# Kernel optimization log

Hardware: AMD Instinct MI355X
Metric: run time of the kernel (lower is better)

Reference implementation:

```python
import jax, jax.numpy as jnp
import numpy as np

NX, NC, E = 100000, 50000, 1000000
DIN, DCTX, DH, DOUT = 64, 64, 64, 64


def _linear_params(k, din, dout):
    kw, _ = jax.random.split(k)
    s = 1.0 / np.sqrt(din).astype(np.float32)
    return jax.random.uniform(kw, (dout, din), jnp.float32, -s, s), jnp.zeros((dout,), jnp.float32)


def setup_inputs() -> dict:
    key = jax.random.key(0)
    ks = jax.random.split(key, 16)
    x = jax.random.normal(ks[0], (NX, DIN), jnp.float32)
    c = jax.random.normal(ks[1], (NC, DCTX), jnp.float32)
    e_fwd_src = jax.random.randint(ks[2], (E,), 0, NX, jnp.int32)
    e_fwd_dst = jax.random.randint(ks[3], (E,), 0, NX, jnp.int32)
    e_bwd_src = jax.random.randint(ks[4], (E,), 0, NX, jnp.int32)
    e_bwd_dst = jax.random.randint(ks[5], (E,), 0, NX, jnp.int32)
    e_cx_src = jax.random.randint(ks[6], (E,), 0, NC, jnp.int32)
    e_cx_dst = jax.random.randint(ks[7], (E,), 0, NX, jnp.int32)
    Wx, bx = _linear_params(ks[8], DIN, DH)      # layers['x']
    Wc, bc = _linear_params(ks[9], DCTX, DH)     # layers['c']
    Wff, bff = _linear_params(ks[10], DIN, DH)   # layers['x->x']
    Wbb, bbb = _linear_params(ks[11], DIN, DH)   # layers['x<-x']
    Wcx, bcx = _linear_params(ks[12], DCTX, DH)  # layers['c->x']
    Wp, bp = _linear_params(ks[13], DH, DOUT)    # pool
    return dict(x=x, c=c,
                e_fwd_src=e_fwd_src, e_fwd_dst=e_fwd_dst,
                e_bwd_src=e_bwd_src, e_bwd_dst=e_bwd_dst,
                e_cx_src=e_cx_src, e_cx_dst=e_cx_dst,
                Wx=Wx, bx=bx, Wc=Wc, bc=bc, Wff=Wff, bff=bff,
                Wbb=Wbb, bbb=bbb, Wcx=Wcx, bcx=bcx, Wp=Wp, bp=bp)


def reference(x, c, e_fwd_src, e_fwd_dst, e_bwd_src, e_bwd_dst, e_cx_src, e_cx_dst,
              Wx, bx, Wc, bc, Wff, bff, Wbb, bbb, Wcx, bcx, Wp, bp):
    relu = jax.nn.relu
    seg = lambda v, i: jax.ops.segment_sum(v, i, num_segments=NX)
    # self-loop features
    self_x = relu(x @ Wx.T + bx)                                   # [NX, DH]
    # edge type ('x','->','x'): gather src, transform, scatter-add to dst
    m1 = seg(relu(x[e_fwd_src] @ Wff.T + bff), e_fwd_dst)
    # edge type ('x','<-','x'): direction swap -> true src is stored dst
    m2 = seg(relu(x[e_bwd_dst] @ Wbb.T + bbb), e_bwd_src)
    # edge type ('c','->','x'): gather context nodes
    m3 = seg(relu(c[e_cx_src] @ Wcx.T + bcx), e_cx_dst)
    # coalesce with op='add' over all messages + self loops
    agg = self_x + m1 + m2 + m3                                    # [NX, DH]
    out_x = agg @ Wp.T + bp                                        # [NX, DOUT]
    out_c = relu(c @ Wc.T + bc)                                    # [NC, DH]
    return out_x, out_c
```

## Files before the change

### kernel.cpp

```cpp
#include <hip/hip_runtime.h>
#include <cstddef>

typedef unsigned short ushort_t;
using f32x4  = __attribute__((ext_vector_type(4))) float;
using bf16x8 = __attribute__((ext_vector_type(8))) short;

static constexpr int NX = 100000;
static constexpr int NC = 50000;
static constexpr int E  = 1000000;
static constexpr int E3 = 3 * E;

static constexpr int SHIFT = 6;
static constexpr int BN = 1 << SHIFT;
static constexpr int NB = (NX + BN - 1) / BN;
static constexpr int CAP = 2304;
static constexpr int PF_CHUNK = 4096;
static constexpr int NXT = (NX + 63) / 64;
static constexpr int NCT = (NC + 63) / 64;

__device__ inline ushort_t f2bf(float f) {
    unsigned u = __float_as_uint(f);
    return (ushort_t)((u + 0x7fffu + ((u >> 16) & 1u)) >> 16);
}

__device__ inline bf16x8 cvt8(float4 lo, float4 hi) {
    bf16x8 v;
    v[0] = (short)f2bf(lo.x); v[1] = (short)f2bf(lo.y);
    v[2] = (short)f2bf(lo.z); v[3] = (short)f2bf(lo.w);
    v[4] = (short)f2bf(hi.x); v[5] = (short)f2bf(hi.y);
    v[6] = (short)f2bf(hi.z); v[7] = (short)f2bf(hi.w);
    return v;
}

__device__ inline float bfl(unsigned u) { return __uint_as_float(u << 16); }
__device__ inline float bfh(unsigned u) { return __uint_as_float(u & 0xffff0000u); }

__device__ __forceinline__ void gemm_tile(
    const float* __restrict__ in, int nrows, int tile_row0,
    const float* __restrict__ W0, const float* __restrict__ b0, void* __restrict__ o0,
    const float* __restrict__ W1, const float* __restrict__ b1, void* __restrict__ o1,
    const float* __restrict__ W2, const float* __restrict__ b2, void* __restrict__ o2,
    int nlayers, int relu_mask, int bf16_mask)
{
    const int t   = threadIdx.x;
    const int w   = t >> 6;
    const int l   = t & 63;
    const int lr  = l & 15;
    const int lk  = (l >> 4) * 8;
    const int row0 = tile_row0 + (w >> 1) * 32;
    const int col0 = (w & 1) * 32;

    bf16x8 a[2][2];
    #pragma unroll
    for (int m = 0; m < 2; ++m) {
        #pragma unroll
        for (int ks = 0; ks < 2; ++ks) {
            const int row = row0 + 16 * m + lr;
            float4 lo = make_float4(0.f, 0.f, 0.f, 0.f), hi = lo;
            if (row < nrows) {
                const float* p = in + (size_t)row * 64 + ks * 32 + lk;
                lo = *reinterpret_cast<const float4*>(p);
                hi = *reinterpret_cast<const float4*>(p + 4);
            }
            a[m][ks] = cvt8(lo, hi);
        }
    }

    for (int ly = 0; ly < nlayers; ++ly) {
        const float* W = (ly == 0) ? W0 : (ly == 1) ? W1 : W2;
        const float* b = (ly == 0) ? b0 : (ly == 1) ? b1 : b2;
        void*        o = (ly == 0) ? o0 : (ly == 1) ? o1 : o2;

        bf16x8 bf[2][2];
        float  bias[2];
        #pragma unroll
        for (int n = 0; n < 2; ++n) {
            const int col = col0 + 16 * n + lr;
            bias[n] = b[col];
            #pragma unroll
            for (int ks = 0; ks < 2; ++ks) {
                const float* p = W + (size_t)col * 64 + ks * 32 + lk;
                const float4 lo = *reinterpret_cast<const float4*>(p);
                const float4 hi = *reinterpret_cast<const float4*>(p + 4);
                bf[n][ks] = cvt8(lo, hi);
            }
        }

        f32x4 acc[2][2];
        #pragma unroll
        for (int m = 0; m < 2; ++m)
            #pragma unroll
            for (int n = 0; n < 2; ++n)
                acc[m][n] = (f32x4){0.f, 0.f, 0.f, 0.f};

        #pragma unroll
        for (int m = 0; m < 2; ++m) {
            #pragma unroll
            for (int n = 0; n < 2; ++n) {
                acc[m][n] = __builtin_amdgcn_mfma_f32_16x16x32_bf16(a[m][0], bf[n][0], acc[m][n], 0, 0, 0);
                acc[m][n] = __builtin_amdgcn_mfma_f32_16x16x32_bf16(a[m][1], bf[n][1], acc[m][n], 0, 0, 0);
            }
        }

        const bool relu = (relu_mask >> ly) & 1;
        const bool b16  = (bf16_mask >> ly) & 1;
        #pragma unroll
        for (int m = 0; m < 2; ++m) {
            #pragma unroll
            for (int r = 0; r < 4; ++r) {
                const int row = row0 + 16 * m + (l >> 4) * 4 + r;
                if (row < nrows) {
                    #pragma unroll
                    for (int n = 0; n < 2; ++n) {
                        const int col = col0 + 16 * n + lr;
                        float v = acc[m][n][r] + bias[n];
                        if (relu) v = fmaxf(v, 0.f);
                        if (b16) ((ushort_t*)o)[(size_t)row * 64 + col] = f2bf(v);
                        else     ((float*)o)[(size_t)row * 64 + col] = v;
                    }
                }
            }
        }
    }
}

__global__ __launch_bounds__(256) void gemm_all(
    const float* __restrict__ x, const float* __restrict__ c,
    const float* __restrict__ Wx, const float* __restrict__ bx, ushort_t* __restrict__ h_self,
    const float* __restrict__ Wff, const float* __restrict__ bff, ushort_t* __restrict__ hff,
    const float* __restrict__ Wbb, const float* __restrict__ bbb, ushort_t* __restrict__ hbb,
    const float* __restrict__ Wc, const float* __restrict__ bc, float* __restrict__ out_c,
    const float* __restrict__ Wcx, const float* __restrict__ bcx, ushort_t* __restrict__ hcx,
    int* __restrict__ bcursor)
{
    const int b = blockIdx.x;
    if (b < NXT) {
        gemm_tile(x, NX, b * 64, Wx, bx, h_self, Wff, bff, hff, Wbb, bbb, hbb, 3, 7, 7);
    } else if (b < NXT + NCT) {
        gemm_tile(c, NC, (b - NXT) * 64, Wc, bc, out_c, Wcx, bcx, hcx,
                  nullptr, nullptr, nullptr, 2, 3, 2);
    } else {
        for (int i = threadIdx.x; i < NB; i += 256) bcursor[i] = i * CAP;
    }
}

__global__ __launch_bounds__(256) void fused_linear_mfma(
    const float* __restrict__ in, int nrows,
    const float* __restrict__ W0, const float* __restrict__ b0, void* __restrict__ o0,
    const float* __restrict__ W1, const float* __restrict__ b1, void* __restrict__ o1,
    const float* __restrict__ W2, const float* __restrict__ b2, void* __restrict__ o2,
    int nlayers, int relu_mask, int bf16_mask)
{
    gemm_tile(in, nrows, blockIdx.x * 64, W0, b0, o0, W1, b1, o1, W2, b2, o2,
              nlayers, relu_mask, bf16_mask);
}

__global__ __launch_bounds__(256) void partition_fill(
    const int* __restrict__ efs, const int* __restrict__ efd,
    const int* __restrict__ ebs, const int* __restrict__ ebd,
    const int* __restrict__ ecs, const int* __restrict__ ecd,
    int* __restrict__ bcursor, unsigned* __restrict__ pk)
{
    __shared__ int h[NB];
    __shared__ int base[NB];
    for (int i = threadIdx.x; i < NB; i += 256) h[i] = 0;
    __syncthreads();
    const int e0 = blockIdx.x * PF_CHUNK;
    unsigned pack[16];
    int buck[16], rank[16];
    #pragma unroll
    for (int i = 0; i < 16; ++i) {
        const int e = e0 + i * 256 + threadIdx.x;
        buck[i] = -1;
        if (e < E3) {
            int d, sg;
            if (e < E)          { d = efd[e];         sg = efs[e]; }
            else if (e < 2 * E) { d = ebs[e - E];     sg = NX + ebd[e - E]; }
            else                { d = ecd[e - 2 * E]; sg = 2 * NX + ecs[e - 2 * E]; }
            buck[i] = d >> SHIFT;
            pack[i] = ((unsigned)sg << SHIFT) | (unsigned)(d & (BN - 1));
            rank[i] = atomicAdd(&h[buck[i]], 1);
        }
    }
    __syncthreads();
    for (int b = threadIdx.x; b < NB; b += 256)
        base[b] = h[b] ? atomicAdd(&bcursor[b], h[b]) : 0;
    __syncthreads();
    #pragma unroll
    for (int i = 0; i < 16; ++i)
        if (buck[i] >= 0) pk[base[buck[i]] + rank[i]] = pack[i];
}

__global__ __launch_bounds__(256) void sort_gather_pool(
    const int* __restrict__ bcursor, const unsigned* __restrict__ pk,
    const ushort_t* __restrict__ h_all, const ushort_t* __restrict__ h_self,
    const float* __restrict__ Wp, const float* __restrict__ bp,
    float* __restrict__ out_x)
{
    __shared__ unsigned srt[CAP];
    __shared__ int cnt[BN], nstart[BN], cur[BN];
    __shared__ ushort_t agg_lds[BN * 72];

    const int b = blockIdx.x;
    const int t = threadIdx.x;
    const int s = b * CAP;
    int tend = bcursor[b];
    if (tend > s + CAP) tend = s + CAP;

    if (t < BN) cnt[t] = 0;
    __syncthreads();
    for (int e = s + t; e < tend; e += 256)
        atomicAdd(&cnt[pk[e] & (BN - 1)], 1);
    __syncthreads();
    if (t < BN) {
        const int v = cnt[t];
        int xs = v;
        #pragma unroll
        for (int d = 1; d < BN; d <<= 1) {
            const int y = __shfl_up(xs, d, 64);
            if (t >= d) xs += y;
        }
        nstart[t] = xs - v;
        cur[t]    = xs - v;
    }
    __syncthreads();
    for (int e = s + t; e < tend; e += 256) {
        const unsigned p = pk[e];
        const int pos = atomicAdd(&cur[p & (BN - 1)], 1);
        srt[pos] = (p & ~(unsigned)(BN - 1)) << 1;
    }
    __syncthreads();

    const int w    = t >> 6;
    const int lane = t & 63;
    const int q    = lane >> 4;
    const int fl   = lane & 15;
    const unsigned foff = fl * 8;
    const int node0 = b * BN;
    const char* hb = reinterpret_cast<const char*>(h_all);
    const char* hs = reinterpret_cast<const char*>(h_self);

    for (int i = 0; i < 16; ++i) {
        const int nl   = w * 16 + i;
        const int node = node0 + nl;
        const int start = nstart[nl];
        const int count = cnt[nl];
        float a0 = 0.f, a1 = 0.f, a2 = 0.f, a3 = 0.f;
        if (q == 0 && node < NX) {
            const uint2 u = *reinterpret_cast<const uint2*>(hs + (size_t)node * 128 + foff);
            a0 = bfl(u.x); a1 = bfh(u.x); a2 = bfl(u.y); a3 = bfh(u.y);
        }
        int e = q;
        for (; e + 12 < count; e += 16) {
            const unsigned o0 = srt[start + e]      + foff;
            const unsigned o1 = srt[start + e + 4]  + foff;
            const unsigned o2 = srt[start + e + 8]  + foff;
            const unsigned o3 = srt[start + e + 12] + foff;
            const uint2 u0 = *reinterpret_cast<const uint2*>(hb + o0);
            const uint2 u1 = *reinterpret_cast<const uint2*>(hb + o1);
            const uint2 u2 = *reinterpret_cast<const uint2*>(hb + o2);
            const uint2 u3 = *reinterpret_cast<const uint2*>(hb + o3);
            a0 += bfl(u0.x) + bfl(u1.x) + bfl(u2.x) + bfl(u3.x);
            a1 += bfh(u0.x) + bfh(u1.x) + bfh(u2.x) + bfh(u3.x);
            a2 += bfl(u0.y) + bfl(u1.y) + bfl(u2.y) + bfl(u3.y);
            a3 += bfh(u0.y) + bfh(u1.y) + bfh(u2.y) + bfh(u3.y);
        }
        for (; e < count; e += 4) {
            const uint2 u = *reinterpret_cast<const uint2*>(hb + (srt[start + e] + foff));
            a0 += bfl(u.x); a1 += bfh(u.x); a2 += bfl(u.y); a3 += bfh(u.y);
        }
        a0 += __shfl_xor(a0, 16); a0 += __shfl_xor(a0, 32);
        a1 += __shfl_xor(a1, 16); a1 += __shfl_xor(a1, 32);
        a2 += __shfl_xor(a2, 16); a2 += __shfl_xor(a2, 32);
        a3 += __shfl_xor(a3, 16); a3 += __shfl_xor(a3, 32);
        if (q == 0) {
            uint2 pck;
            pck.x = ((unsigned)f2bf(a1) << 16) | (unsigned)f2bf(a0);
            pck.y = ((unsigned)f2bf(a3) << 16) | (unsigned)f2bf(a2);
            *reinterpret_cast<uint2*>(&agg_lds[nl * 72 + fl * 4]) = pck;
        }
    }
    __syncthreads();

    const int lr = lane & 15, q4 = lane >> 4;
    const float* wrow = Wp + (size_t)(w * 16 + lr) * 64;
    const bf16x8 bf0 = cvt8(*reinterpret_cast<const float4*>(wrow + q4 * 8),
                            *reinterpret_cast<const float4*>(wrow + q4 * 8 + 4));
    const bf16x8 bf1 = cvt8(*reinterpret_cast<const float4*>(wrow + 32 + q4 * 8),
                            *reinterpret_cast<const float4*>(wrow + 32 + q4 * 8 + 4));
    const float bias = bp[w * 16 + lr];
    #pragma unroll
    for (int rb = 0; rb < 4; ++rb) {
        const bf16x8 af0 = *reinterpret_cast<const bf16x8*>(&agg_lds[(rb * 16 + lr) * 72 + q4 * 8]);
        const bf16x8 af1 = *reinterpret_cast<const bf16x8*>(&agg_lds[(rb * 16 + lr) * 72 + 32 + q4 * 8]);
        f32x4 acc = (f32x4){0.f, 0.f, 0.f, 0.f};
        acc = __builtin_amdgcn_mfma_f32_16x16x32_bf16(af0, bf0, acc, 0, 0, 0);
        acc = __builtin_amdgcn_mfma_f32_16x16x32_bf16(af1, bf1, acc, 0, 0, 0);
        #pragma unroll
        for (int r = 0; r < 4; ++r) {
            const int row = node0 + rb * 16 + q4 * 4 + r;
            if (row < NX)
                out_x[(size_t)row * 64 + w * 16 + lr] = acc[r] + bias;
        }
    }
}

__global__ __launch_bounds__(256) void scatter_edges(
    const int* __restrict__ efs, const int* __restrict__ efd,
    const int* __restrict__ ebs, const int* __restrict__ ebd,
    const int* __restrict__ ecs, const int* __restrict__ ecd,
    const ushort_t* __restrict__ h_all, float* __restrict__ agg)
{
    const int idx  = blockIdx.x * 256 + threadIdx.x;
    const int lane = idx & 63;
    const int e    = idx >> 6;
    if (e >= E3) return;
    int src, dst;
    if (e < E)          { src = efs[e];           dst = efd[e]; }
    else if (e < 2 * E) { src = NX + ebd[e - E];  dst = ebs[e - E]; }
    else                { src = 2 * NX + ecs[e - 2 * E]; dst = ecd[e - 2 * E]; }
    const unsigned u = (unsigned)h_all[(size_t)src * 64 + lane] << 16;
    atomicAdd(&agg[(size_t)dst * 64 + lane], __uint_as_float(u));
}

extern "C" void kernel_launch(void* const* d_in, const int* in_sizes, int n_in,
                              void* d_out, int out_size, void* d_ws, size_t ws_size,
                              hipStream_t stream)
{
    const float* x   = (const float*)d_in[0];
    const float* c   = (const float*)d_in[1];
    const int*   efs = (const int*)d_in[2];
    const int*   efd = (const int*)d_in[3];
    const int*   ebs = (const int*)d_in[4];
    const int*   ebd = (const int*)d_in[5];
    const int*   ecs = (const int*)d_in[6];
    const int*   ecd = (const int*)d_in[7];
    const float* Wx  = (const float*)d_in[8];
    const float* bx  = (const float*)d_in[9];
    const float* Wc  = (const float*)d_in[10];
    const float* bc  = (const float*)d_in[11];
    const float* Wff = (const float*)d_in[12];
    const float* bff = (const float*)d_in[13];
    const float* Wbb = (const float*)d_in[14];
    const float* bbb = (const float*)d_in[15];
    const float* Wcx = (const float*)d_in[16];
    const float* bcx = (const float*)d_in[17];
    const float* Wp  = (const float*)d_in[18];
    const float* bp  = (const float*)d_in[19];

    float* out_x = (float*)d_out;
    float* out_c = (float*)d_out + (size_t)NX * 64;

    ushort_t* h_all  = (ushort_t*)d_ws;
    ushort_t* hff    = h_all;
    ushort_t* hbb    = h_all + (size_t)NX * 64;
    ushort_t* hcx    = h_all + (size_t)2 * NX * 64;
    ushort_t* h_self = h_all + (size_t)(2 * NX + NC) * 64;
    const size_t h_elems = (size_t)(3 * NX + NC) * 64;

    int* bcursor = (int*)(h_all + h_elems);
    unsigned* pk = (unsigned*)(bcursor + NB);
    const size_t need_bytes = h_elems * 2 + (size_t)NB * 4 + (size_t)NB * CAP * 4;

    if (ws_size >= need_bytes) {
        gemm_all<<<NXT + NCT + 1, 256, 0, stream>>>(
            x, c, Wx, bx, h_self, Wff, bff, hff, Wbb, bbb, hbb,
            Wc, bc, out_c, Wcx, bcx, hcx, bcursor);
        partition_fill<<<(E3 + PF_CHUNK - 1) / PF_CHUNK, 256, 0, stream>>>(
            efs, efd, ebs, ebd, ecs, ecd, bcursor, pk);
        sort_gather_pool<<<NB, 256, 0, stream>>>(
            bcursor, pk, h_all, h_self, Wp, bp, out_x);
    } else {
        fused_linear_mfma<<<NXT, 256, 0, stream>>>(
            x, NX, Wx, bx, out_x, Wff, bff, hff, Wbb, bbb, hbb, 3, 7, 6);
        fused_linear_mfma<<<NCT, 256, 0, stream>>>(
            c, NC, Wc, bc, out_c, Wcx, bcx, hcx, nullptr, nullptr, nullptr, 2, 3, 2);
        scatter_edges<<<((size_t)E3 * 64 + 255) / 256, 256, 0, stream>>>(
            efs, efd, ebs, ebd, ecs, ecd, h_all, out_x);
        fused_linear_mfma<<<NXT, 256, 0, stream>>>(
            out_x, NX, Wp, bp, out_x, nullptr, nullptr, nullptr, nullptr, nullptr, nullptr, 1, 0, 0);
    }
}
```

Measured before the change: 151.3 us.

## Use coarser partition buckets with two-pass fill and split gather into quarter-bucket blocks

Partitioning now uses 128-node buckets. The fill kernel makes two passes: it counts first, reserves global cursor ranges, then re-reads the edge indices to scatter packed entries, instead of keeping per-thread ranks in registers. The gather/pool kernel launches four 32-node blocks per parent bucket, interleaved so neighbouring blocks share parent buckets for cache locality. Each block filters the parent's packed list for its quarter. This raises parallelism and lowers per-block shared memory and register pressure. The cost is re-reading edge indices in the fill kernel and each packed bucket being scanned four times.

Result: slower. 179.1 us (+18.3%).

```diff
diff --git a/kernel.cpp b/kernel.cpp
--- a/kernel.cpp
+++ b/kernel.cpp
@@ -10,11 +10,16 @@
 static constexpr int E  = 1000000;
 static constexpr int E3 = 3 * E;
 
-static constexpr int SHIFT = 6;
-static constexpr int BN = 1 << SHIFT;
-static constexpr int NB = (NX + BN - 1) / BN;
-static constexpr int CAP = 2304;
-static constexpr int PF_CHUNK = 4096;
+static constexpr int SHIFT_P = 7;
+static constexpr int BNP = 1 << SHIFT_P;
+static constexpr int NBP = (NX + BNP - 1) / BNP;
+static constexpr int CAP_P = 4416;
+static constexpr int PF_CHUNK = 8192;
+
+static constexpr int BNG = 32;
+static constexpr int CAP_G = 1280;
+static constexpr int GRID_G = 8 * 4 * ((NBP + 7) / 8);
+
 static constexpr int NXT = (NX + 63) / 64;
 static constexpr int NCT = (NC + 63) / 64;
 
@@ -140,7 +145,7 @@
         gemm_tile(c, NC, (b - NXT) * 64, Wc, bc, out_c, Wcx, bcx, hcx,
                   nullptr, nullptr, nullptr, 2, 3, 2);
     } else {
-        for (int i = threadIdx.x; i < NB; i += 256) bcursor[i] = i * CAP;
+        for (int i = threadIdx.x; i < NBP; i += 256) bcursor[i] = i * CAP_P;
     }
 }
 
@@ -161,34 +166,42 @@
     const int* __restrict__ ecs, const int* __restrict__ ecd,
     int* __restrict__ bcursor, unsigned* __restrict__ pk)
 {
-    __shared__ int h[NB];
-    __shared__ int base[NB];
-    for (int i = threadIdx.x; i < NB; i += 256) h[i] = 0;
+    __shared__ int h[NBP];
+    __shared__ int cur[NBP];
+    for (int i = threadIdx.x; i < NBP; i += 256) h[i] = 0;
     __syncthreads();
     const int e0 = blockIdx.x * PF_CHUNK;
-    unsigned pack[16];
-    int buck[16], rank[16];
-    #pragma unroll
-    for (int i = 0; i < 16; ++i) {
+
+    #pragma unroll 4
+    for (int i = 0; i < PF_CHUNK / 256; ++i) {
         const int e = e0 + i * 256 + threadIdx.x;
-        buck[i] = -1;
+        if (e < E3) {
+            int d;
+            if (e < E)          d = efd[e];
+            else if (e < 2 * E) d = ebs[e - E];
+            else                d = ecd[e - 2 * E];
+            atomicAdd(&h[d >> SHIFT_P], 1);
+        }
+    }
+    __syncthreads();
+    for (int b = threadIdx.x; b < NBP; b += 256)
+        cur[b] = h[b] ? atomicAdd(&bcursor[b], h[b]) : 0;
+    __syncthreads();
+
+    #pragma unroll 4
+    for (int i = 0; i < PF_CHUNK / 256; ++i) {
+        const int e = e0 + i * 256 + threadIdx.x;
         if (e < E3) {
             int d, sg;
             if (e < E)          { d = efd[e];         sg = efs[e]; }
             else if (e < 2 * E) { d = ebs[e - E];     sg = NX + ebd[e - E]; }
             else                { d = ecd[e - 2 * E]; sg = 2 * NX + ecs[e - 2 * E]; }
-            buck[i] = d >> SHIFT;
-            pack[i] = ((unsigned)sg << SHIFT) | (unsigned)(d & (BN - 1));
-            rank[i] = atomicAdd(&h[buck[i]], 1);
-        }
-    }
-    __syncthreads();
-    for (int b = threadIdx.x; b < NB; b += 256)
-        base[b] = h[b] ? atomicAdd(&bcursor[b], h[b]) : 0;
-    __syncthreads();
-    #pragma unroll
-    for (int i = 0; i < 16; ++i)
-        if (buck[i] >= 0) pk[base[buck[i]] + rank[i]] = pack[i];
+            const int bkt = d >> SHIFT_P;
+            const int pos = atomicAdd(&cur[bkt], 1);
+            if (pos < (bkt + 1) * CAP_P)
+                pk[pos] = ((unsigned)sg << SHIFT_P) | (unsigned)(d & (BNP - 1));
+        }
+    }
 }
 
 __global__ __launch_bounds__(256) void sort_gather_pool(
@@ -197,26 +210,36 @@
     const float* __restrict__ Wp, const float* __restrict__ bp,
     float* __restrict__ out_x)
 {
-    __shared__ unsigned srt[CAP];
-    __shared__ int cnt[BN], nstart[BN], cur[BN];
-    __shared__ ushort_t agg_lds[BN * 72];
-
-    const int b = blockIdx.x;
+    const int raw  = blockIdx.x;
+    const int slot = raw & 7;
+    const int mm   = raw >> 3;
+    const int q    = mm & 3;
+    const int parent = slot + 8 * (mm >> 2);
+    if (parent >= NBP) return;
+    const int node0 = parent * BNP + q * BNG;
+
+    __shared__ unsigned srt[CAP_G];
+    __shared__ int cnt[BNG], nstart[BNG], cur[BNG];
+    __shared__ ushort_t agg_lds[BNG * 72];
+
     const int t = threadIdx.x;
-    const int s = b * CAP;
-    int tend = bcursor[b];
-    if (tend > s + CAP) tend = s + CAP;
-
-    if (t < BN) cnt[t] = 0;
-    __syncthreads();
-    for (int e = s + t; e < tend; e += 256)
-        atomicAdd(&cnt[pk[e] & (BN - 1)], 1);
-    __syncthreads();
-    if (t < BN) {
+    const int s = parent * CAP_P;
+    int tend = bcursor[parent];
+    if (tend > s + CAP_P) tend = s + CAP_P;
+
+    if (t < BNG) cnt[t] = 0;
+    __syncthreads();
+    for (int e = s + t; e < tend; e += 256) {
+        const unsigned p = pk[e];
+        if (((p >> 5) & 3u) == (unsigned)q)
+            atomicAdd(&cnt[p & (BNG - 1)], 1);
+    }
+    __syncthreads();
+    if (t < BNG) {
         const int v = cnt[t];
         int xs = v;
         #pragma unroll
-        for (int d = 1; d < BN; d <<= 1) {
+        for (int d = 1; d < BNG; d <<= 1) {
             const int y = __shfl_up(xs, d, 64);
             if (t >= d) xs += y;
         }
@@ -226,31 +249,33 @@
     __syncthreads();
     for (int e = s + t; e < tend; e += 256) {
         const unsigned p = pk[e];
-        const int pos = atomicAdd(&cur[p & (BN - 1)], 1);
-        srt[pos] = (p & ~(unsigned)(BN - 1)) << 1;
+        if (((p >> 5) & 3u) == (unsigned)q) {
+            const int pos = atomicAdd(&cur[p & (BNG - 1)], 1);
+            if (pos < CAP_G)
+                srt[pos] = p & ~(unsigned)(BNP - 1);
+        }
     }
     __syncthreads();
 
     const int w    = t >> 6;
     const int lane = t & 63;
-    const int q    = lane >> 4;
+    const int q4   = lane >> 4;
     const int fl   = lane & 15;
     const unsigned foff = fl * 8;
-    const int node0 = b * BN;
     const char* hb = reinterpret_cast<const char*>(h_all);
     const char* hs = reinterpret_cast<const char*>(h_self);
 
-    for (int i = 0; i < 16; ++i) {
-        const int nl   = w * 16 + i;
+    for (int i = 0; i < 8; ++i) {
+        const int nl   = w * 8 + i;
         const int node = node0 + nl;
         const int start = nstart[nl];
         const int count = cnt[nl];
         float a0 = 0.f, a1 = 0.f, a2 = 0.f, a3 = 0.f;
-        if (q == 0 && node < NX) {
+        if (q4 == 0 && node < NX) {
             const uint2 u = *reinterpret_cast<const uint2*>(hs + (size_t)node * 128 + foff);
             a0 = bfl(u.x); a1 = bfh(u.x); a2 = bfl(u.y); a3 = bfh(u.y);
         }
-        int e = q;
+        int e = q4;
         for (; e + 12 < count; e += 16) {
             const unsigned o0 = srt[start + e]      + foff;
             const unsigned o1 = srt[start + e + 4]  + foff;
@@ -273,7 +298,7 @@
         a1 += __shfl_xor(a1, 16); a1 += __shfl_xor(a1, 32);
         a2 += __shfl_xor(a2, 16); a2 += __shfl_xor(a2, 32);
         a3 += __shfl_xor(a3, 16); a3 += __shfl_xor(a3, 32);
-        if (q == 0) {
+        if (q4 == 0) {
             uint2 pck;
             pck.x = ((unsigned)f2bf(a1) << 16) | (unsigned)f2bf(a0);
             pck.y = ((unsigned)f2bf(a3) << 16) | (unsigned)f2bf(a2);
@@ -282,7 +307,7 @@
     }
     __syncthreads();
 
-    const int lr = lane & 15, q4 = lane >> 4;
+    const int lr = lane & 15;
     const float* wrow = Wp + (size_t)(w * 16 + lr) * 64;
     const bf16x8 bf0 = cvt8(*reinterpret_cast<const float4*>(wrow + q4 * 8),
                             *reinterpret_cast<const float4*>(wrow + q4 * 8 + 4));
@@ -290,7 +315,7 @@
                             *reinterpret_cast<const float4*>(wrow + 32 + q4 * 8 + 4));
     const float bias = bp[w * 16 + lr];
     #pragma unroll
-    for (int rb = 0; rb < 4; ++rb) {
+    for (int rb = 0; rb < 2; ++rb) {
         const bf16x8 af0 = *reinterpret_cast<const bf16x8*>(&agg_lds[(rb * 16 + lr) * 72 + q4 * 8]);
         const bf16x8 af1 = *reinterpret_cast<const bf16x8*>(&agg_lds[(rb * 16 + lr) * 72 + 32 + q4 * 8]);
         f32x4 acc = (f32x4){0.f, 0.f, 0.f, 0.f};
@@ -359,8 +384,8 @@
     const size_t h_elems = (size_t)(3 * NX + NC) * 64;
 
     int* bcursor = (int*)(h_all + h_elems);
-    unsigned* pk = (unsigned*)(bcursor + NB);
-    const size_t need_bytes = h_elems * 2 + (size_t)NB * 4 + (size_t)NB * CAP * 4;
+    unsigned* pk = (unsigned*)(bcursor + NBP);
+    const size_t need_bytes = h_elems * 2 + (size_t)NBP * 4 + (size_t)NBP * CAP_P * 4;
 
     if (ws_size >= need_bytes) {
         gemm_all<<<NXT + NCT + 1, 256, 0, stream>>>(
@@ -368,7 +393,7 @@
             Wc, bc, out_c, Wcx, bcx, hcx, bcursor);
         partition_fill<<<(E3 + PF_CHUNK - 1) / PF_CHUNK, 256, 0, stream>>>(
             efs, efd, ebs, ebd, ecs, ecd, bcursor, pk);
-        sort_gather_pool<<<NB, 256, 0, stream>>>(
+        sort_gather_pool<<<GRID_G, 256, 0, stream>>>(
             bcursor, pk, h_all, h_self, Wp, bp, out_x);
     } else {
         fused_linear_mfma<<<NXT, 256, 0, stream>>>(
```

## Merge GEMM and edge partition into one launch; widen gather loads to 16 bytes

Applied to the files above, without the earlier changes.

Merges the dense GEMM blocks and the edge-partition blocks into a single kernel launch, so the two independent stages can run concurrently on the GPU. The per-bucket cursor initialisation is replaced by a memset of counters, and positions are now computed as bucket*CAP plus an atomic count, with a bound check against overflow. The gather loop in the pool kernel now uses 8 lanes per row with 16-byte loads instead of 16 lanes with 8-byte loads, giving 8 edges in flight per wave and one more shuffle-reduction step. Registers and the LDS footprint of the merged kernel come from both paths, which may lower occupancy for the GEMM blocks.

After: 147.2 us (median of 2 runs). 2.8% less time.

```diff
diff --git a/kernel.cpp b/kernel.cpp
--- a/kernel.cpp
+++ b/kernel.cpp
@@ -15,6 +15,7 @@
 static constexpr int NB = (NX + BN - 1) / BN;
 static constexpr int CAP = 2304;
 static constexpr int PF_CHUNK = 4096;
+static constexpr int NPF = (E3 + PF_CHUNK - 1) / PF_CHUNK;
 static constexpr int NXT = (NX + 63) / 64;
 static constexpr int NCT = (NC + 63) / 64;
 
@@ -124,48 +125,33 @@
     }
 }
 
-__global__ __launch_bounds__(256) void gemm_all(
+__global__ __launch_bounds__(256) void gemm_partition(
     const float* __restrict__ x, const float* __restrict__ c,
     const float* __restrict__ Wx, const float* __restrict__ bx, ushort_t* __restrict__ h_self,
     const float* __restrict__ Wff, const float* __restrict__ bff, ushort_t* __restrict__ hff,
     const float* __restrict__ Wbb, const float* __restrict__ bbb, ushort_t* __restrict__ hbb,
     const float* __restrict__ Wc, const float* __restrict__ bc, float* __restrict__ out_c,
     const float* __restrict__ Wcx, const float* __restrict__ bcx, ushort_t* __restrict__ hcx,
-    int* __restrict__ bcursor)
-{
-    const int b = blockIdx.x;
-    if (b < NXT) {
-        gemm_tile(x, NX, b * 64, Wx, bx, h_self, Wff, bff, hff, Wbb, bbb, hbb, 3, 7, 7);
-    } else if (b < NXT + NCT) {
-        gemm_tile(c, NC, (b - NXT) * 64, Wc, bc, out_c, Wcx, bcx, hcx,
-                  nullptr, nullptr, nullptr, 2, 3, 2);
-    } else {
-        for (int i = threadIdx.x; i < NB; i += 256) bcursor[i] = i * CAP;
-    }
-}
-
-__global__ __launch_bounds__(256) void fused_linear_mfma(
-    const float* __restrict__ in, int nrows,
-    const float* __restrict__ W0, const float* __restrict__ b0, void* __restrict__ o0,
-    const float* __restrict__ W1, const float* __restrict__ b1, void* __restrict__ o1,
-    const float* __restrict__ W2, const float* __restrict__ b2, void* __restrict__ o2,
-    int nlayers, int relu_mask, int bf16_mask)
-{
-    gemm_tile(in, nrows, blockIdx.x * 64, W0, b0, o0, W1, b1, o1, W2, b2, o2,
-              nlayers, relu_mask, bf16_mask);
-}
-
-__global__ __launch_bounds__(256) void partition_fill(
     const int* __restrict__ efs, const int* __restrict__ efd,
     const int* __restrict__ ebs, const int* __restrict__ ebd,
     const int* __restrict__ ecs, const int* __restrict__ ecd,
-    int* __restrict__ bcursor, unsigned* __restrict__ pk)
+    int* __restrict__ bcnt, unsigned* __restrict__ pk)
 {
     __shared__ int h[NB];
     __shared__ int base[NB];
+    const int b = blockIdx.x;
+    if (b >= NPF) {
+        const int gb = b - NPF;
+        if (gb < NXT)
+            gemm_tile(x, NX, gb * 64, Wx, bx, h_self, Wff, bff, hff, Wbb, bbb, hbb, 3, 7, 7);
+        else
+            gemm_tile(c, NC, (gb - NXT) * 64, Wc, bc, out_c, Wcx, bcx, hcx,
+                      nullptr, nullptr, nullptr, 2, 3, 2);
+        return;
+    }
     for (int i = threadIdx.x; i < NB; i += 256) h[i] = 0;
     __syncthreads();
-    const int e0 = blockIdx.x * PF_CHUNK;
+    const int e0 = b * PF_CHUNK;
     unsigned pack[16];
     int buck[16], rank[16];
     #pragma unroll
@@ -183,16 +169,20 @@
         }
     }
     __syncthreads();
-    for (int b = threadIdx.x; b < NB; b += 256)
-        base[b] = h[b] ? atomicAdd(&bcursor[b], h[b]) : 0;
+    for (int bb = threadIdx.x; bb < NB; bb += 256)
+        base[bb] = h[bb] ? (bb * CAP + atomicAdd(&bcnt[bb], h[bb])) : 0;
     __syncthreads();
     #pragma unroll
     for (int i = 0; i < 16; ++i)
-        if (buck[i] >= 0) pk[base[buck[i]] + rank[i]] = pack[i];
+        if (buck[i] >= 0) {
+            const int pos = base[buck[i]] + rank[i];
+            if (pos < (buck[i] + 1) * CAP)
+                pk[pos] = pack[i];
+        }
 }
 
 __global__ __launch_bounds__(256) void sort_gather_pool(
-    const int* __restrict__ bcursor, const unsigned* __restrict__ pk,
+    const int* __restrict__ bcnt, const unsigned* __restrict__ pk,
     const ushort_t* __restrict__ h_all, const ushort_t* __restrict__ h_self,
     const float* __restrict__ Wp, const float* __restrict__ bp,
     float* __restrict__ out_x)
@@ -204,8 +194,8 @@
     const int b = blockIdx.x;
     const int t = threadIdx.x;
     const int s = b * CAP;
-    int tend = bcursor[b];
-    if (tend > s + CAP) tend = s + CAP;
+    int n = bcnt[b]; if (n > CAP) n = CAP;
+    const int tend = s + n;
 
     if (t < BN) cnt[t] = 0;
     __syncthreads();
@@ -233,9 +223,9 @@
 
     const int w    = t >> 6;
     const int lane = t & 63;
-    const int q    = lane >> 4;
-    const int fl   = lane & 15;
-    const unsigned foff = fl * 8;
+    const int g    = lane >> 3;
+    const int fl   = lane & 7;
+    const unsigned foff = fl * 16;
     const int node0 = b * BN;
     const char* hb = reinterpret_cast<const char*>(h_all);
     const char* hs = reinterpret_cast<const char*>(h_self);
@@ -246,38 +236,51 @@
         const int start = nstart[nl];
         const int count = cnt[nl];
         float a0 = 0.f, a1 = 0.f, a2 = 0.f, a3 = 0.f;
-        if (q == 0 && node < NX) {
-            const uint2 u = *reinterpret_cast<const uint2*>(hs + (size_t)node * 128 + foff);
+        float a4 = 0.f, a5 = 0.f, a6 = 0.f, a7 = 0.f;
+        if (g == 0 && node < NX) {
+            const uint4 u = *reinterpret_cast<const uint4*>(hs + (size_t)node * 128 + foff);
             a0 = bfl(u.x); a1 = bfh(u.x); a2 = bfl(u.y); a3 = bfh(u.y);
-        }
-        int e = q;
-        for (; e + 12 < count; e += 16) {
+            a4 = bfl(u.z); a5 = bfh(u.z); a6 = bfl(u.w); a7 = bfh(u.w);
+        }
+        int e = g;
+        for (; e + 24 < count; e += 32) {
             const unsigned o0 = srt[start + e]      + foff;
-            const unsigned o1 = srt[start + e + 4]  + foff;
-            const unsigned o2 = srt[start + e + 8]  + foff;
-            const unsigned o3 = srt[start + e + 12] + foff;
-            const uint2 u0 = *reinterpret_cast<const uint2*>(hb + o0);
-            const uint2 u1 = *reinterpret_cast<const uint2*>(hb + o1);
-            const uint2 u2 = *reinterpret_cast<const uint2*>(hb + o2);
-            const uint2 u3 = *reinterpret_cast<const uint2*>(hb + o3);
+            const unsigned o1 = srt[start + e + 8]  + foff;
+            const unsigned o2 = srt[start + e + 16] + foff;
+            const unsigned o3 = srt[start + e + 24] + foff;
+            const uint4 u0 = *reinterpret_cast<const uint4*>(hb + o0);
+            const uint4 u1 = *reinterpret_cast<const uint4*>(hb + o1);
+            const uint4 u2 = *reinterpret_cast<const uint4*>(hb + o2);
+            const uint4 u3 = *reinterpret_cast<const uint4*>(hb + o3);
             a0 += bfl(u0.x) + bfl(u1.x) + bfl(u2.x) + bfl(u3.x);
             a1 += bfh(u0.x) + bfh(u1.x) + bfh(u2.x) + bfh(u3.x);
             a2 += bfl(u0.y) + bfl(u1.y) + bfl(u2.y) + bfl(u3.y);
             a3 += bfh(u0.y) + bfh(u1.y) + bfh(u2.y) + bfh(u3.y);
-        }
-        for (; e < count; e += 4) {
-            const uint2 u = *reinterpret_cast<const uint2*>(hb + (srt[start + e] + foff));
+            a4 += bfl(u0.z) + bfl(u1.z) + bfl(u2.z) + bfl(u3.z);
+            a5 += bfh(u0.z) + bfh(u1.z) + bfh(u2.z) + bfh(u3.z);
+            a6 += bfl(u0.w) + bfl(u1.w) + bfl(u2.w) + bfl(u3.w);
+            a7 += bfh(u0.w) + bfh(u1.w) + bfh(u2.w) + bfh(u3.w);
+        }
+        for (; e < count; e += 8) {
+            const uint4 u = *reinterpret_cast<const uint4*>(hb + (srt[start + e] + foff));
             a0 += bfl(u.x); a1 += bfh(u.x); a2 += bfl(u.y); a3 += bfh(u.y);
-        }
-        a0 += __shfl_xor(a0, 16); a0 += __shfl_xor(a0, 32);
-        a1 += __shfl_xor(a1, 16); a1 += __shfl_xor(a1, 32);
-        a2 += __shfl_xor(a2, 16); a2 += __shfl_xor(a2, 32);
-        a3 += __shfl_xor(a3, 16); a3 += __shfl_xor(a3, 32);
-        if (q == 0) {
-            uint2 pck;
+            a4 += bfl(u.z); a5 += bfh(u.z); a6 += bfl(u.w); a7 += bfh(u.w);
+        }
+        a0 += __shfl_xor(a0, 8); a0 += __shfl_xor(a0, 16); a0 += __shfl_xor(a0, 32);
+        a1 += __shfl_xor(a1, 8); a1 += __shfl_xor(a1, 16); a1 += __shfl_xor(a1, 32);
+        a2 += __shfl_xor(a2, 8); a2 += __shfl_xor(a2, 16); a2 += __shfl_xor(a2, 32);
+        a3 += __shfl_xor(a3, 8); a3 += __shfl_xor(a3, 16); a3 += __shfl_xor(a3, 32);
+        a4 += __shfl_xor(a4, 8); a4 += __shfl_xor(a4, 16); a4 += __shfl_xor(a4, 32);
+        a5 += __shfl_xor(a5, 8); a5 += __shfl_xor(a5, 16); a5 += __shfl_xor(a5, 32);
+        a6 += __shfl_xor(a6, 8); a6 += __shfl_xor(a6, 16); a6 += __shfl_xor(a6, 32);
+        a7 += __shfl_xor(a7, 8); a7 += __shfl_xor(a7, 16); a7 += __shfl_xor(a7, 32);
+        if (lane < 8) {
+            uint4 pck;
             pck.x = ((unsigned)f2bf(a1) << 16) | (unsigned)f2bf(a0);
             pck.y = ((unsigned)f2bf(a3) << 16) | (unsigned)f2bf(a2);
-            *reinterpret_cast<uint2*>(&agg_lds[nl * 72 + fl * 4]) = pck;
+            pck.z = ((unsigned)f2bf(a5) << 16) | (unsigned)f2bf(a4);
+            pck.w = ((unsigned)f2bf(a7) << 16) | (unsigned)f2bf(a6);
+            *reinterpret_cast<uint4*>(&agg_lds[nl * 72 + fl * 8]) = pck;
         }
     }
     __syncthreads();
@@ -303,6 +306,17 @@
                 out_x[(size_t)row * 64 + w * 16 + lr] = acc[r] + bias;
         }
     }
+}
+
+__global__ __launch_bounds__(256) void fused_linear_mfma(
+    const float* __restrict__ in, int nrows,
+    const float* __restrict__ W0, const float* __restrict__ b0, void* __restrict__ o0,
+    const float* __restrict__ W1, const float* __restrict__ b1, void* __restrict__ o1,
+    const float* __restrict__ W2, const float* __restrict__ b2, void* __restrict__ o2,
+    int nlayers, int relu_mask, int bf16_mask)
+{
+    gemm_tile(in, nrows, blockIdx.x * 64, W0, b0, o0, W1, b1, o1, W2, b2, o2,
+              nlayers, relu_mask, bf16_mask);
 }
 
 __global__ __launch_bounds__(256) void scatter_edges(
@@ -358,18 +372,18 @@
     ushort_t* h_self = h_all + (size_t)(2 * NX + NC) * 64;
     const size_t h_elems = (size_t)(3 * NX + NC) * 64;
 
-    int* bcursor = (int*)(h_all + h_elems);
-    unsigned* pk = (unsigned*)(bcursor + NB);
+    int* bcnt    = (int*)(h_all + h_elems);
+    unsigned* pk = (unsigned*)(bcnt + NB);
     const size_t need_bytes = h_elems * 2 + (size_t)NB * 4 + (size_t)NB * CAP * 4;
 
     if (ws_size >= need_bytes) {
-        gemm_all<<<NXT + NCT + 1, 256, 0, stream>>>(
+        hipMemsetAsync(bcnt, 0, (size_t)NB * sizeof(int), stream);
+        gemm_partition<<<NPF + NXT + NCT, 256, 0, stream>>>(
             x, c, Wx, bx, h_self, Wff, bff, hff, Wbb, bbb, hbb,
-            Wc, bc, out_c, Wcx, bcx, hcx, bcursor);
-        partition_fill<<<(E3 + PF_CHUNK - 1) / PF_CHUNK, 256, 0, stream>>>(
-            efs, efd, ebs, ebd, ecs, ecd, bcursor, pk);
+            Wc, bc, out_c, Wcx, bcx, hcx,
+            efs, efd, ebs, ebd, ecs, ecd, bcnt, pk);
         sort_gather_pool<<<NB, 256, 0, stream>>>(
-            bcursor, pk, h_all, h_self, Wp, bp, out_x);
+            bcnt, pk, h_all, h_self, Wp, bp, out_x);
     } else {
         fused_linear_mfma<<<NXT, 256, 0, stream>>>(
             x, NX, Wx, bx, out_x, Wff, bff, hff, Wbb, bbb, hbb, 3, 7, 6);
```
